# Kernel optimization log

Measured on AMD Instinct MI355X. Metric: run time of the kernel, lower is better.

## Reference

```python
import jax, jax.numpy as jnp
import numpy as np

B, K, C, D, L, H, FF = 64, 1024, 512, 256, 2, 4, 1024
DH = D // H
EPS = 1e-5
NEG = -jnp.inf
SCALE = 1.0 / float(np.sqrt(DH))


def _ln(x, w, b):
    m = x.mean(-1, keepdims=True)
    v = ((x - m) ** 2).mean(-1, keepdims=True)
    return (x - m) * jax.lax.rsqrt(v + EPS) * w + b


def _star_attn(x, key_pad, pad_c, Wq, bq, Wk, bk, Wv, bv, Wo, bo):
    # Star topology: rows 0,1 (query,dustbin) attend to all non-padded keys;
    # each candidate row attends only to {query, dustbin, itself}.
    Bb, S, _ = x.shape
    q = (x @ Wq.T + bq).reshape(Bb, S, H, DH)
    k = (x @ Wk.T + bk).reshape(Bb, S, H, DH)
    v = (x @ Wv.T + bv).reshape(Bb, S, H, DH)
    # global rows
    qg = q[:, :2]
    sg = jnp.einsum('bthd,bshd->bhts', qg, k) * SCALE            # [B,H,2,S]
    sg = jnp.where(key_pad[:, None, None, :], NEG, sg)
    out_g = jnp.einsum('bhts,bshd->bthd', jax.nn.softmax(sg, -1), v)  # [B,2,H,DH]
    # candidate rows: scores against the 2 global keys + self key
    qc, kc, vc = q[:, 2:], k[:, 2:], v[:, 2:]
    kg, vg = k[:, :2], v[:, :2]
    s2 = jnp.einsum('bkhd,bthd->bkht', qc, kg) * SCALE           # [B,K,H,2]
    ss = jnp.einsum('bkhd,bkhd->bkh', qc, kc) * SCALE            # [B,K,H]
    ss = jnp.where(pad_c[:, :, None], NEG, ss)                   # padded self-key disallowed
    w = jax.nn.softmax(jnp.concatenate([s2, ss[..., None]], -1), -1)  # [B,K,H,3]
    out_c = jnp.einsum('bkht,bthd->bkhd', w[..., :2], vg) + w[..., 2:] * vc
    out = jnp.concatenate([out_g, out_c], 1).reshape(Bb, S, D)
    return out @ Wo.T + bo


def _forward(query, candidates, candidate_mask, qp_w, qp_b, cp_w, cp_b,
             dustbin, type_emb, ln1_w, ln1_b, ln2_w, ln2_b,
             Wq, bq, Wk, bk, Wv, bv, Wo, bo,
             ff1_w, ff1_b, ff2_w, ff2_b, head_ln_w, head_ln_b, head_w, head_b):
    Bb = query.shape[0]
    qt = (query @ qp_w.T + qp_b + type_emb[0])[:, None]          # [B,1,D]
    dt = jnp.broadcast_to(dustbin + type_emb[1], (Bb, 1, D))
    ct = candidates @ cp_w.T + cp_b + type_emb[2]                # [B,K,D]
    x = jnp.concatenate([qt, dt, ct], 1)                         # [B,K+2,D]
    pad_c = jnp.logical_not(candidate_mask)
    key_pad = jnp.concatenate([jnp.zeros((Bb, 2), bool), pad_c], 1)
    for l in range(L):  # pre-LN encoder layers (norm_first, eval so dropout=0)
        x = x + _star_attn(_ln(x, ln1_w[l], ln1_b[l]), key_pad, pad_c,
                           Wq[l], bq[l], Wk[l], bk[l], Wv[l], bv[l], Wo[l], bo[l])
        h = _ln(x, ln2_w[l], ln2_b[l])
        x = x + (jax.nn.gelu(h @ ff1_w[l].T + ff1_b[l], approximate=False) @ ff2_w[l].T + ff2_b[l])
    logits = (_ln(x, head_ln_w, head_ln_b) @ head_w.T + head_b)[..., 0]  # [B,K+2]
    cand = jnp.where(candidate_mask, logits[:, 2:], NEG)
    return jnp.concatenate([logits[:, 1:2], cand], 1)            # [B,K+1]


def setup_inputs() -> dict:
    key = jax.random.key(0)
    ks = iter(jax.random.split(key, 40))
    n = lambda shape, s=0.02: jax.random.normal(next(ks), shape, jnp.float32) * s
    return dict(
        query=jax.random.normal(next(ks), (B, C), jnp.float32),
        candidates=jax.random.normal(next(ks), (B, K, C), jnp.float32),
        candidate_mask=jax.random.bernoulli(next(ks), 0.9, (B, K)),
        qp_w=n((D, C)), qp_b=jnp.zeros(D),
        cp_w=n((D, C)), cp_b=jnp.zeros(D),
        dustbin=n((D,)), type_emb=n((3, D)),
        ln1_w=jnp.ones((L, D)), ln1_b=jnp.zeros((L, D)),
        ln2_w=jnp.ones((L, D)), ln2_b=jnp.zeros((L, D)),
        Wq=n((L, D, D)), bq=jnp.zeros((L, D)),
        Wk=n((L, D, D)), bk=jnp.zeros((L, D)),
        Wv=n((L, D, D)), bv=jnp.zeros((L, D)),
        Wo=n((L, D, D)), bo=jnp.zeros((L, D)),
        ff1_w=n((L, FF, D)), ff1_b=jnp.zeros((L, FF)),
        ff2_w=n((L, D, FF)), ff2_b=jnp.zeros((L, D)),
        head_ln_w=jnp.ones(D), head_ln_b=jnp.zeros(D),
        head_w=n((1, D)), head_b=jnp.zeros(1),
    )


def reference(query, candidates, candidate_mask, qp_w, qp_b, cp_w, cp_b,
              dustbin, type_emb, ln1_w, ln1_b, ln2_w, ln2_b,
              Wq, bq, Wk, bk, Wv, bv, Wo, bo,
              ff1_w, ff1_b, ff2_w, ff2_b, head_ln_w, head_ln_b, head_w, head_b):
    return _forward(query, candidates, candidate_mask, qp_w, qp_b, cp_w, cp_b,
                    dustbin, type_emb, ln1_w, ln1_b, ln2_w, ln2_b,
                    Wq, bq, Wk, bk, Wv, bv, Wo, bo,
                    ff1_w, ff1_b, ff2_w, ff2_b, head_ln_w, head_ln_b, head_w, head_b)
```

## Files before the change

kernel.cpp:

```cpp
#include <hip/hip_runtime.h>
#include <math.h>

static constexpr int Bc = 64;
static constexpr int Kc = 1024;
static constexpr int Cc = 512;
static constexpr int Dc = 256;
static constexpr int Hc = 4;
static constexpr int Sc = 1026;
static constexpr int FFc = 1024;
static constexpr float EPSc = 1e-5f;
static constexpr float SCALEc = 0.125f;
static constexpr float NEG_OUT = -1.0e30f;

typedef __attribute__((ext_vector_type(8))) short short8;
typedef __attribute__((ext_vector_type(8))) unsigned short u16x8;
typedef __attribute__((ext_vector_type(4))) float f32x4;

__device__ __forceinline__ float bf2f(unsigned short u) {
  union { float f; unsigned int i; } c; c.i = ((unsigned int)u) << 16; return c.f;
}
__device__ __forceinline__ unsigned short f2bf(float f) {
  union { float f; unsigned int i; } c; c.f = f;
  unsigned int i = c.i;
  unsigned int r = (i + 0x7fffu + ((i >> 16) & 1u)) >> 16;
  return (unsigned short)r;
}
__device__ __forceinline__ unsigned int cvt_pk_bf16(float a, float b) {
  unsigned int d;
  asm("v_cvt_pk_bf16_f32 %0, %1, %2" : "=v"(d) : "v"(a), "v"(b));
  return d;
}

__device__ __forceinline__ float wave_sum(float v) {
#pragma unroll
  for (int off = 32; off > 0; off >>= 1) v += __shfl_xor(v, off, 64);
  return v;
}
__device__ __forceinline__ float wave_max(float v) {
#pragma unroll
  for (int off = 32; off > 0; off >>= 1) v = fmaxf(v, __shfl_xor(v, off, 64));
  return v;
}

__device__ __forceinline__ void async_ld16(const unsigned short* g, unsigned short* l) {
  __builtin_amdgcn_global_load_lds(
      (const __attribute__((address_space(1))) void*)g,
      (__attribute__((address_space(3))) void*)l, 16, 0, 0);
}

__device__ __forceinline__ float gelu_fast(float u) {
  const float z = 1.5957691216057308f * u * (1.0f + 0.044715f * u * u);
  return u / (1.0f + __expf(-z));
}

template <int EPI, int MAP, int CASTA>
__global__ __launch_bounds__(256) void gemm_mfma(
    const void* __restrict__ Av, const unsigned short* __restrict__ W,
    const float* __restrict__ bias, const void* extra,
    void* Cout, int N, int Kd, int ldc, int MB, int NB) {
  __shared__ unsigned short lds[16384];
  const int xcd = blockIdx.x & 7;
  const int slot = blockIdx.x >> 3;
  const int nb = slot % NB;
  const int mb = (slot / NB) * 8 + xcd;
  if (mb >= MB) return;
  const int m0 = mb * 128;
  const int n0 = nb * 128;
  const int tid = threadIdx.x;
  const int w = tid >> 6;
  const int lane = tid & 63;

  const unsigned short* A = (const unsigned short*)Av;
  const float* Af = (const float*)Av;

  const int srA[2] = {(w * 2 + 0) * 16 + (lane >> 2), (w * 2 + 1) * 16 + (lane >> 2)};
  const unsigned short* pA[2];
  const unsigned short* pB[2];
#pragma unroll
  for (int c = 0; c < 2; ++c) {
    const int kc = ((lane & 3) ^ ((srA[c] >> 1) & 3)) * 8;
    if (!CASTA) pA[c] = A + (size_t)(m0 + srA[c]) * Kd + kc;
    pB[c] = W + (size_t)(n0 + srA[c]) * Kd + kc;
  }
  const int lreg0 = (w * 2 + 0) * 512;
  const int lreg1 = (w * 2 + 1) * 512;

  f32x4 zero = {0.f, 0.f, 0.f, 0.f};
  f32x4 acc[4][4];
#pragma unroll
  for (int i = 0; i < 4; ++i)
#pragma unroll
    for (int j = 0; j < 4; ++j) acc[i][j] = zero;

  const int mrow = (w & 1) * 64;
  const int nrow = (w >> 1) * 64;
  const int l15 = lane & 15;
  const int quad = lane >> 4;
  const int koff = (quad ^ ((l15 >> 1) & 3)) * 16;

  auto stage = [&](int kk, int b) {
    if (CASTA) {
#pragma unroll
      for (int wi = 0; wi < 4; ++wi) {
        const int g = wi * 256 + tid;
        const int row = g >> 3;
        const int k4 = g & 7;
        const int phys =
            row * 32 + ((((k4 >> 1) ^ ((row >> 1) & 3))) << 3) + ((k4 & 1) << 2);
        const float4 a4 =
            *(const float4*)(Af + (size_t)(m0 + row) * Kd + kk + k4 * 4);
        uint2 o;
        o.x = cvt_pk_bf16(a4.x, a4.y);
        o.y = cvt_pk_bf16(a4.z, a4.w);
        *(uint2*)(&lds[b * 4096 + phys]) = o;
      }
    } else {
      async_ld16(pA[0] + kk, &lds[b * 4096 + lreg0]);
      async_ld16(pA[1] + kk, &lds[b * 4096 + lreg1]);
    }
    async_ld16(pB[0] + kk, &lds[8192 + b * 4096 + lreg0]);
    async_ld16(pB[1] + kk, &lds[8192 + b * 4096 + lreg1]);
  };

  const int niter = Kd >> 5;
  stage(0, 0);
  for (int it = 0; it < niter; ++it) {
    const int cur = it & 1;
    __syncthreads();
    if (it + 1 < niter) stage((it + 1) << 5, cur ^ 1);
    const char* AsB = (const char*)&lds[cur * 4096];
    const char* WsB = (const char*)&lds[8192 + cur * 4096];
    short8 af[4], bfr[4];
#pragma unroll
    for (int i = 0; i < 4; ++i)
      af[i] = *(const short8*)(AsB + (size_t)(mrow + i * 16 + l15) * 64 + koff);
#pragma unroll
    for (int j = 0; j < 4; ++j)
      bfr[j] = *(const short8*)(WsB + (size_t)(nrow + j * 16 + l15) * 64 + koff);
#pragma unroll
    for (int i = 0; i < 4; ++i)
#pragma unroll
      for (int j = 0; j < 4; ++j)
        acc[i][j] = __builtin_amdgcn_mfma_f32_16x16x32_bf16(bfr[j], af[i],
                                                            acc[i][j], 0, 0, 0);
  }

  const float* extraF = (const float*)extra;
  const unsigned short* extraB = (const unsigned short*)extra;
  float4 bj[4];
#pragma unroll
  for (int j = 0; j < 4; ++j) {
    const int n = n0 + nrow + j * 16 + quad * 4;
    float4 t4 = *(const float4*)(bias + n);
    if (EPI == 1) {
      const float4 e4 = *(const float4*)(extraF + n);
      t4.x += e4.x; t4.y += e4.y; t4.z += e4.z; t4.w += e4.w;
    }
    bj[j] = t4;
  }
  __syncthreads();
#pragma unroll
  for (int i = 0; i < 4; ++i) {
    const int m = mrow + i * 16 + l15;
    const int swz = (m & 7) << 1;
#pragma unroll
    for (int j = 0; j < 4; ++j) {
      float v0 = acc[i][j][0] + bj[j].x;
      float v1 = acc[i][j][1] + bj[j].y;
      float v2 = acc[i][j][2] + bj[j].z;
      float v3 = acc[i][j][3] + bj[j].w;
      if (EPI == 3) {
        v0 = gelu_fast(v0); v1 = gelu_fast(v1);
        v2 = gelu_fast(v2); v3 = gelu_fast(v3);
      }
      uint2 pk;
      pk.x = cvt_pk_bf16(v0, v1);
      pk.y = cvt_pk_bf16(v2, v3);
      const int g = ((nrow + j * 16 + quad * 4) >> 2) ^ swz;
      *(uint2*)(&lds[m * 128 + g * 4]) = pk;
    }
  }
  __syncthreads();
  unsigned short* outb = (unsigned short*)Cout;
#pragma unroll
  for (int c8 = 0; c8 < 8; ++c8) {
    const int idx = c8 * 256 + tid;
    const int row = idx >> 4;
    const int cc = idx & 15;
    const int gsr = (2 * cc) ^ ((row & 7) << 1);
    u16x8 val = *(const u16x8*)(&lds[row * 128 + gsr * 4]);
    const int col = cc * 8;
    const int m = m0 + row;
    const size_t orow =
        (MAP == 1) ? ((size_t)(m >> 10) * Sc + 2 + (m & 1023)) : (size_t)m;
    const size_t go = orow * (size_t)ldc + n0 + col;
    if (EPI == 2) {
      u16x8 rv = *(const u16x8*)(extraB + go);
      unsigned int* vp = (unsigned int*)&val;
#pragma unroll
      for (int e = 0; e < 4; ++e) {
        const float a0 = bf2f(val[2 * e]) + bf2f(rv[2 * e]);
        const float a1 = bf2f(val[2 * e + 1]) + bf2f(rv[2 * e + 1]);
        vp[e] = cvt_pk_bf16(a0, a1);
      }
    }
    *(u16x8*)(outb + go) = val;
  }
}

struct CastTab {
  const float* src[10];
  unsigned short* dst[10];
  int n4[10];
};
__global__ __launch_bounds__(256) void cast_multi(CastTab t) {
  const int e = blockIdx.y;
  const int n4 = t.n4[e];
  const float4* s = (const float4*)t.src[e];
  uint2* d = (uint2*)t.dst[e];
  for (int i = blockIdx.x * 256 + threadIdx.x; i < n4; i += gridDim.x * 256) {
    float4 f = s[i];
    uint2 o;
    o.x = cvt_pk_bf16(f.x, f.y);
    o.y = cvt_pk_bf16(f.z, f.w);
    d[i] = o;
  }
}

__global__ __launch_bounds__(256) void bias_concat(const float* bq, const float* bk,
                                                   const float* bv, float* qkvb) {
  const int i = blockIdx.x * 256 + threadIdx.x;
  if (i >= 2 * 768) return;
  const int l = i / 768;
  const int j = i - l * 768;
  float v;
  if (j < 256) v = bq[l * 256 + j];
  else if (j < 512) v = bk[l * 256 + j - 256];
  else v = bv[l * 256 + j - 512];
  qkvb[i] = v;
}

__global__ __launch_bounds__(256) void embed_qd(
    const float* __restrict__ qin, const float* __restrict__ qp_w,
    const float* __restrict__ qp_b, const float* __restrict__ dustbin,
    const float* __restrict__ type_emb, unsigned short* __restrict__ x) {
  const int b = blockIdx.x;
  const int d = threadIdx.x;
  __shared__ __align__(16) float qs[512];
  qs[d] = qin[b * 512 + d];
  qs[d + 256] = qin[b * 512 + 256 + d];
  __syncthreads();
  float acc = 0.0f;
  const float* wr = qp_w + (size_t)d * 512;
#pragma unroll 4
  for (int c = 0; c < 512; c += 4) {
    float4 w4 = *(const float4*)(wr + c);
    acc = fmaf(qs[c], w4.x, acc);
    acc = fmaf(qs[c + 1], w4.y, acc);
    acc = fmaf(qs[c + 2], w4.z, acc);
    acc = fmaf(qs[c + 3], w4.w, acc);
  }
  const size_t base = (size_t)b * Sc * Dc;
  x[base + d] = f2bf(acc + qp_b[d] + type_emb[d]);
  x[base + Dc + d] = f2bf(dustbin[d] + type_emb[Dc + d]);
}

__global__ __launch_bounds__(256) void ln_kernel(
    const unsigned short* __restrict__ x, const float* __restrict__ w,
    const float* __restrict__ b, unsigned short* __restrict__ y, int nrows) {
  const int wave = threadIdx.x >> 6;
  const int lane = threadIdx.x & 63;
  const int row = blockIdx.x * 4 + wave;
  if (row >= nrows) return;
  const unsigned short* xr = x + (size_t)row * Dc;
  ushort4 xv = *(const ushort4*)(xr + lane * 4);
  const float v0 = bf2f(xv.x), v1 = bf2f(xv.y), v2 = bf2f(xv.z), v3 = bf2f(xv.w);
  float s = v0 + v1 + v2 + v3;
  float sq = v0 * v0 + v1 * v1 + v2 * v2 + v3 * v3;
  s = wave_sum(s);
  sq = wave_sum(sq);
  const float mean = s * (1.0f / Dc);
  const float var = sq * (1.0f / Dc) - mean * mean;
  const float rs = rsqrtf(var + EPSc);
  float4 wv = *(const float4*)(w + lane * 4);
  float4 bv = *(const float4*)(b + lane * 4);
  uint2 o;
  o.x = cvt_pk_bf16((v0 - mean) * rs * wv.x + bv.x,
                    (v1 - mean) * rs * wv.y + bv.y);
  o.y = cvt_pk_bf16((v2 - mean) * rs * wv.z + bv.z,
                    (v3 - mean) * rs * wv.w + bv.w);
  *(uint2*)(y + (size_t)row * Dc + lane * 4) = o;
}

__global__ __launch_bounds__(256) void attn_global(
    const unsigned short* __restrict__ qkv, const unsigned char* __restrict__ mask,
    unsigned short* __restrict__ ao) {
  const int b = blockIdx.x;
  const int h = blockIdx.y;
  const int tid = threadIdx.x;
  const int wv = tid >> 6;
  const int lane = tid & 63;
  __shared__ float q0s[64], q1s[64];
  __shared__ float sc0[Sc], sc1[Sc];
  __shared__ float rbuf[4][2];
  __shared__ float obuf[2][4][64];
  const size_t base = (size_t)b * Sc * 768 + h * 64;
  if (tid < 64) {
    q0s[tid] = bf2f(qkv[base + tid]);
    q1s[tid] = bf2f(qkv[base + 768 + tid]);
  }
  __syncthreads();

  float lm0 = -INFINITY, lm1 = -INFINITY;
  for (int s = tid; s < Sc; s += 256) {
    const unsigned short* kr = qkv + base + 256 + (size_t)s * 768;
    float d0 = 0.0f, d1 = 0.0f;
#pragma unroll
    for (int c = 0; c < 64; c += 8) {
      u16x8 kv = *(const u16x8*)(kr + c);
#pragma unroll
      for (int e = 0; e < 8; ++e) {
        const float kf = bf2f(kv[e]);
        d0 = fmaf(q0s[c + e], kf, d0);
        d1 = fmaf(q1s[c + e], kf, d1);
      }
    }
    const bool pad = (s >= 2) && (mask[b * Kc + (s - 2)] == 0);
    const float s0 = pad ? -INFINITY : d0 * SCALEc;
    const float s1 = pad ? -INFINITY : d1 * SCALEc;
    sc0[s] = s0; sc1[s] = s1;
    lm0 = fmaxf(lm0, s0); lm1 = fmaxf(lm1, s1);
  }
  lm0 = wave_max(lm0);
  lm1 = wave_max(lm1);
  if (lane == 0) { rbuf[wv][0] = lm0; rbuf[wv][1] = lm1; }
  __syncthreads();
  const float m0 = fmaxf(fmaxf(rbuf[0][0], rbuf[1][0]), fmaxf(rbuf[2][0], rbuf[3][0]));
  const float m1 = fmaxf(fmaxf(rbuf[0][1], rbuf[1][1]), fmaxf(rbuf[2][1], rbuf[3][1]));
  float ls0 = 0.0f, ls1 = 0.0f;
  for (int s = tid; s < Sc; s += 256) {
    const float e0 = expf(sc0[s] - m0);
    const float e1 = expf(sc1[s] - m1);
    sc0[s] = e0; sc1[s] = e1;
    ls0 += e0; ls1 += e1;
  }
  ls0 = wave_sum(ls0);
  ls1 = wave_sum(ls1);
  __syncthreads();
  if (lane == 0) { rbuf[wv][0] = ls0; rbuf[wv][1] = ls1; }
  __syncthreads();
  const float t0 = rbuf[0][0] + rbuf[1][0] + rbuf[2][0] + rbuf[3][0];
  const float t1 = rbuf[0][1] + rbuf[1][1] + rbuf[2][1] + rbuf[3][1];
  float o0 = 0.0f, o1 = 0.0f;
  for (int s = wv; s < Sc; s += 4) {
    const float vvv = bf2f(qkv[base + 512 + (size_t)s * 768 + lane]);
    o0 = fmaf(sc0[s], vvv, o0);
    o1 = fmaf(sc1[s], vvv, o1);
  }
  obuf[0][wv][lane] = o0;
  obuf[1][wv][lane] = o1;
  __syncthreads();
  if (wv == 0) {
    const float a0 = obuf[0][0][lane] + obuf[0][1][lane] + obuf[0][2][lane] + obuf[0][3][lane];
    const float a1 = obuf[1][0][lane] + obuf[1][1][lane] + obuf[1][2][lane] + obuf[1][3][lane];
    const size_t ob = ((size_t)b * Sc) * Dc + h * 64;
    ao[ob + lane] = f2bf(a0 / t0);
    ao[ob + Dc + lane] = f2bf(a1 / t1);
  }
}

__global__ __launch_bounds__(256) void attn_cand(
    const unsigned short* __restrict__ qkv, const unsigned char* __restrict__ mask,
    unsigned short* __restrict__ ao) {
  const int bk = blockIdx.x;
  const int b = bk >> 10;
  const int kk = bk & 1023;
  const int h = threadIdx.x >> 6;
  const int lane = threadIdx.x & 63;
  const size_t rowg = (size_t)b * Sc * 768 + h * 64;
  const size_t rowc = rowg + (size_t)(2 + kk) * 768;
  const float qc = bf2f(qkv[rowc + lane]);
  float p0 = qc * bf2f(qkv[rowg + 256 + lane]);
  float p1 = qc * bf2f(qkv[rowg + 256 + 768 + lane]);
  float p2 = qc * bf2f(qkv[rowc + 256 + lane]);
#pragma unroll
  for (int off = 32; off > 0; off >>= 1) {
    p0 += __shfl_xor(p0, off, 64);
    p1 += __shfl_xor(p1, off, 64);
    p2 += __shfl_xor(p2, off, 64);
  }
  const bool pad = (mask[b * Kc + kk] == 0);
  const float s0 = p0 * SCALEc;
  const float s1 = p1 * SCALEc;
  const float s2 = pad ? -INFINITY : p2 * SCALEc;
  const float m = fmaxf(fmaxf(s0, s1), s2);
  const float e0 = expf(s0 - m);
  const float e1 = expf(s1 - m);
  const float e2 = pad ? 0.0f : expf(s2 - m);
  const float inv = 1.0f / (e0 + e1 + e2);
  const float o = (e0 * bf2f(qkv[rowg + 512 + lane]) +
                   e1 * bf2f(qkv[rowg + 512 + 768 + lane]) +
                   e2 * bf2f(qkv[rowc + 512 + lane])) * inv;
  ao[((size_t)b * Sc + 2 + kk) * Dc + h * 64 + lane] = f2bf(o);
}

__global__ __launch_bounds__(256) void head_kernel(
    const unsigned short* __restrict__ x, const float* __restrict__ lnw,
    const float* __restrict__ lnb, const float* __restrict__ hw,
    const float* __restrict__ hb, const unsigned char* __restrict__ mask,
    float* __restrict__ out) {
  const int gw = blockIdx.x * 4 + (threadIdx.x >> 6);
  const int lane = threadIdx.x & 63;
  if (gw >= Bc * 1025) return;
  const int b = gw / 1025;
  const int j = gw - b * 1025;
  const int s = 1 + j;
  const unsigned short* xr = x + ((size_t)b * Sc + s) * Dc;
  ushort4 xv = *(const ushort4*)(xr + lane * 4);
  const float v0 = bf2f(xv.x), v1 = bf2f(xv.y), v2 = bf2f(xv.z), v3 = bf2f(xv.w);
  float su = v0 + v1 + v2 + v3;
  float sq = v0 * v0 + v1 * v1 + v2 * v2 + v3 * v3;
  su = wave_sum(su);
  sq = wave_sum(sq);
  const float mean = su * (1.0f / Dc);
  const float var = sq * (1.0f / Dc) - mean * mean;
  const float rs = rsqrtf(var + EPSc);
  float4 wv = *(const float4*)(lnw + lane * 4);
  float4 bv = *(const float4*)(lnb + lane * 4);
  float4 hv = *(const float4*)(hw + lane * 4);
  float d = ((v0 - mean) * rs * wv.x + bv.x) * hv.x +
            ((v1 - mean) * rs * wv.y + bv.y) * hv.y +
            ((v2 - mean) * rs * wv.z + bv.z) * hv.z +
            ((v3 - mean) * rs * wv.w + bv.w) * hv.w;
  d = wave_sum(d);
  if (lane == 0) {
    const float logit = d + hb[0];
    float res;
    if (j == 0) res = logit;
    else res = (mask[b * Kc + (j - 1)] != 0) ? logit : NEG_OUT;
    out[(size_t)b * 1025 + j] = res;
  }
}

extern "C" void kernel_launch(void* const* d_in, const int* in_sizes, int n_in,
                              void* d_out, int out_size, void* d_ws,
                              size_t ws_size, hipStream_t stream) {
  const float* query = (const float*)d_in[0];
  const float* cands = (const float*)d_in[1];
  const unsigned char* mask = (const unsigned char*)d_in[2];
  const float* qp_w = (const float*)d_in[3];
  const float* qp_b = (const float*)d_in[4];
  const float* cp_w = (const float*)d_in[5];
  const float* cp_b = (const float*)d_in[6];
  const float* dustbin = (const float*)d_in[7];
  const float* type_emb = (const float*)d_in[8];
  const float* ln1_w = (const float*)d_in[9];
  const float* ln1_b = (const float*)d_in[10];
  const float* ln2_w = (const float*)d_in[11];
  const float* ln2_b = (const float*)d_in[12];
  const float* Wq = (const float*)d_in[13];
  const float* bq = (const float*)d_in[14];
  const float* Wk = (const float*)d_in[15];
  const float* bk = (const float*)d_in[16];
  const float* Wv = (const float*)d_in[17];
  const float* bv = (const float*)d_in[18];
  const float* Wo = (const float*)d_in[19];
  const float* bo = (const float*)d_in[20];
  const float* f1w = (const float*)d_in[21];
  const float* f1b = (const float*)d_in[22];
  const float* f2w = (const float*)d_in[23];
  const float* f2b = (const float*)d_in[24];
  const float* hlw = (const float*)d_in[25];
  const float* hlb = (const float*)d_in[26];
  const float* hw = (const float*)d_in[27];
  const float* hb = (const float*)d_in[28];
  float* out = (float*)d_out;

  const size_t XSZ = (size_t)Bc * Sc * Dc;
  const size_t FFSZ = (size_t)Bc * Sc * FFc;

  char* p = (char*)d_ws;
  unsigned short* x = (unsigned short*)p;   p += XSZ * 2;
  unsigned short* y = (unsigned short*)p;   p += XSZ * 2;
  unsigned short* ao = (unsigned short*)p;  p += XSZ * 2;
  unsigned short* big = (unsigned short*)p; p += FFSZ * 2;
  unsigned short* qkv = big;
  unsigned short* ff = big;
  unsigned short* cpw_b = (unsigned short*)p;
  unsigned short* qkvw_b = cpw_b + 131072;
  unsigned short* Wo_b = qkvw_b + 2 * 768 * 256;
  unsigned short* f1_b = Wo_b + 131072;
  unsigned short* f2_b = f1_b + 524288;
  float* qkvb = (float*)(f2_b + 524288);

  const int BS = Bc * Sc;
  auto sgrid = [](int MB, int NB) { return (unsigned)(NB * (((MB + 7) >> 3) << 3)); };

  CastTab t;
  t.src[0] = cp_w;  t.dst[0] = cpw_b; t.n4[0] = 131072 / 4;
  t.src[1] = Wo;    t.dst[1] = Wo_b;  t.n4[1] = 131072 / 4;
  t.src[2] = f1w;   t.dst[2] = f1_b;  t.n4[2] = 524288 / 4;
  t.src[3] = f2w;   t.dst[3] = f2_b;  t.n4[3] = 524288 / 4;
  for (int l = 0; l < 2; ++l) {
    t.src[4 + l * 3 + 0] = Wq + l * 65536;
    t.src[4 + l * 3 + 1] = Wk + l * 65536;
    t.src[4 + l * 3 + 2] = Wv + l * 65536;
    t.dst[4 + l * 3 + 0] = qkvw_b + l * 196608 + 0 * 65536;
    t.dst[4 + l * 3 + 1] = qkvw_b + l * 196608 + 1 * 65536;
    t.dst[4 + l * 3 + 2] = qkvw_b + l * 196608 + 2 * 65536;
    t.n4[4 + l * 3 + 0] = 65536 / 4;
    t.n4[4 + l * 3 + 1] = 65536 / 4;
    t.n4[4 + l * 3 + 2] = 65536 / 4;
  }
  cast_multi<<<dim3(128, 10), 256, 0, stream>>>(t);
  bias_concat<<<6, 256, 0, stream>>>(bq, bk, bv, qkvb);

  gemm_mfma<1, 1, 1><<<sgrid(512, 2), 256, 0, stream>>>(
      cands, cpw_b, cp_b, type_emb + 2 * Dc, x, Dc, Cc, Dc, 512, 2);
  embed_qd<<<Bc, 256, 0, stream>>>(query, qp_w, qp_b, dustbin, type_emb, x);

  for (int l = 0; l < 2; ++l) {
    ln_kernel<<<BS / 4, 256, 0, stream>>>(x, ln1_w + l * Dc, ln1_b + l * Dc, y, BS);
    gemm_mfma<4, 0, 0><<<sgrid(513, 6), 256, 0, stream>>>(
        y, qkvw_b + l * 196608, qkvb + l * 768, nullptr, qkv, 768, Dc, 768, 513, 6);
    attn_global<<<dim3(Bc, Hc), 256, 0, stream>>>(qkv, mask, ao);
    attn_cand<<<Bc * Kc, 256, 0, stream>>>(qkv, mask, ao);
    gemm_mfma<2, 0, 0><<<sgrid(513, 2), 256, 0, stream>>>(
        ao, Wo_b + l * 65536, bo + l * Dc, x, x, Dc, Dc, Dc, 513, 2);
    ln_kernel<<<BS / 4, 256, 0, stream>>>(x, ln2_w + l * Dc, ln2_b + l * Dc, y, BS);
    gemm_mfma<3, 0, 0><<<sgrid(513, 8), 256, 0, stream>>>(
        y, f1_b + l * 524288 / 2, f1b + l * FFc, nullptr, ff, FFc, Dc, FFc, 513, 8);
    gemm_mfma<2, 0, 0><<<sgrid(513, 2), 256, 0, stream>>>(
        ff, f2_b + l * 524288 / 2, f2b + l * Dc, x, x, Dc, FFc, Dc, 513, 2);
  }

  head_kernel<<<(Bc * 1025 + 3) / 4, 256, 0, stream>>>(x, hlw, hlb, hw, hb, mask, out);
}
```

Before: 1.037 ms.

## Fuse FF1+GELU+FF2 into one kernel keeping hidden activations in LDS

Result: slower. 1.773 ms (+71.0%).

```diff
diff --git a/kernel.cpp b/kernel.cpp
--- a/kernel.cpp
+++ b/kernel.cpp
@@ -49,8 +49,8 @@
 }
 
 __device__ __forceinline__ float gelu_fast(float u) {
-  const float z = 1.5957691216057308f * u * (1.0f + 0.044715f * u * u);
-  return u / (1.0f + __expf(-z));
+  const float z = u * fmaf(u * u, 0.07135481627f, 1.5957691216f);
+  return __fdividef(u, 1.0f + __expf(-z));
 }
 
 template <int EPI, int MAP, int CASTA>
@@ -205,6 +205,125 @@
       }
     }
     *(u16x8*)(outb + go) = val;
+  }
+}
+
+__global__ __launch_bounds__(512, 2) void ff_fused(
+    const unsigned short* __restrict__ A,
+    const unsigned short* __restrict__ W1,
+    const float* __restrict__ b1,
+    const unsigned short* __restrict__ W2,
+    const float* __restrict__ b2,
+    unsigned short* __restrict__ X) {
+  __shared__ __align__(16) unsigned short hbuf[2][128 * 64];
+  const int m0 = blockIdx.x * 128;
+  const int tid = threadIdx.x;
+  const int w = tid >> 6;
+  const int lane = tid & 63;
+  const int l15 = lane & 15;
+  const int quad = lane >> 4;
+  const int wm = w >> 1;
+  const int wn = w & 1;
+
+  short8 areg[2][8];
+  {
+    const unsigned short* ap0 =
+        A + (size_t)(m0 + wm * 32 + l15) * 256 + quad * 8;
+#pragma unroll
+    for (int i = 0; i < 2; ++i)
+#pragma unroll
+      for (int ks = 0; ks < 8; ++ks)
+        areg[i][ks] = *(const short8*)(ap0 + i * 16 * 256 + ks * 32);
+  }
+
+  const f32x4 zero = {0.f, 0.f, 0.f, 0.f};
+  f32x4 acc2[2][8];
+#pragma unroll
+  for (int i = 0; i < 2; ++i)
+#pragma unroll
+    for (int j = 0; j < 8; ++j) acc2[i][j] = zero;
+
+  const int swz0 = ((wm * 32 + l15) & 7) << 1;
+  const int swz1 = ((wm * 32 + 16 + l15) & 7) << 1;
+
+  for (int c = 0; c < 16; ++c) {
+    f32x4 acc1[2][2];
+#pragma unroll
+    for (int i = 0; i < 2; ++i)
+#pragma unroll
+      for (int j = 0; j < 2; ++j) acc1[i][j] = zero;
+    const unsigned short* w1p =
+        W1 + (size_t)(c * 64 + wn * 32 + l15) * 256 + quad * 8;
+#pragma unroll
+    for (int ks = 0; ks < 8; ++ks) {
+      const short8 wf0 = *(const short8*)(w1p + ks * 32);
+      const short8 wf1 = *(const short8*)(w1p + 16 * 256 + ks * 32);
+      acc1[0][0] = __builtin_amdgcn_mfma_f32_16x16x32_bf16(wf0, areg[0][ks], acc1[0][0], 0, 0, 0);
+      acc1[0][1] = __builtin_amdgcn_mfma_f32_16x16x32_bf16(wf1, areg[0][ks], acc1[0][1], 0, 0, 0);
+      acc1[1][0] = __builtin_amdgcn_mfma_f32_16x16x32_bf16(wf0, areg[1][ks], acc1[1][0], 0, 0, 0);
+      acc1[1][1] = __builtin_amdgcn_mfma_f32_16x16x32_bf16(wf1, areg[1][ks], acc1[1][1], 0, 0, 0);
+    }
+    unsigned short* hb = hbuf[c & 1];
+#pragma unroll
+    for (int i = 0; i < 2; ++i) {
+      const int m = wm * 32 + i * 16 + l15;
+      const int swz = (i == 0) ? swz0 : swz1;
+#pragma unroll
+      for (int j = 0; j < 2; ++j) {
+        const float4 bb =
+            *(const float4*)(b1 + c * 64 + wn * 32 + j * 16 + quad * 4);
+        const float v0 = gelu_fast(acc1[i][j][0] + bb.x);
+        const float v1 = gelu_fast(acc1[i][j][1] + bb.y);
+        const float v2 = gelu_fast(acc1[i][j][2] + bb.z);
+        const float v3 = gelu_fast(acc1[i][j][3] + bb.w);
+        uint2 pk;
+        pk.x = cvt_pk_bf16(v0, v1);
+        pk.y = cvt_pk_bf16(v2, v3);
+        const int g = ((wn * 32 + j * 16 + quad * 4) >> 2) ^ swz;
+        *(uint2*)(&hb[m * 64 + g * 4]) = pk;
+      }
+    }
+    __syncthreads();
+    const unsigned short* w2p =
+        W2 + (size_t)(wn * 128 + l15) * 1024 + c * 64 + quad * 8;
+#pragma unroll
+    for (int ks2 = 0; ks2 < 2; ++ks2) {
+      short8 hf[2];
+#pragma unroll
+      for (int i = 0; i < 2; ++i) {
+        const int m = wm * 32 + i * 16 + l15;
+        const int swz = (i == 0) ? swz0 : swz1;
+        const int g = ((ks2 * 32 + quad * 8) >> 2) ^ swz;
+        hf[i] = *(const short8*)(&hb[m * 64 + g * 4]);
+      }
+#pragma unroll
+      for (int j = 0; j < 8; ++j) {
+        const short8 wf2 = *(const short8*)(w2p + (size_t)(j * 16) * 1024 + ks2 * 32);
+#pragma unroll
+        for (int i = 0; i < 2; ++i)
+          acc2[i][j] = __builtin_amdgcn_mfma_f32_16x16x32_bf16(wf2, hf[i], acc2[i][j], 0, 0, 0);
+      }
+    }
+  }
+
+#pragma unroll
+  for (int i = 0; i < 2; ++i) {
+    const int m = m0 + wm * 32 + i * 16 + l15;
+    unsigned short* xr = X + (size_t)m * 256 + wn * 128;
+#pragma unroll
+    for (int j = 0; j < 8; ++j) {
+      const int n = j * 16 + quad * 4;
+      const float4 bb = *(const float4*)(b2 + wn * 128 + n);
+      const uint2 rv = *(const uint2*)(xr + n);
+      const float v0 = acc2[i][j][0] + bb.x + bf2f((unsigned short)(rv.x & 0xffff));
+      const float v1 = acc2[i][j][1] + bb.y + bf2f((unsigned short)(rv.x >> 16));
+      const float v2 = acc2[i][j][2] + bb.z + bf2f((unsigned short)(rv.y & 0xffff));
+      const float v3 = acc2[i][j][3] + bb.w + bf2f((unsigned short)(rv.y >> 16));
+      uint2 pk;
+      pk.x = cvt_pk_bf16(v0, v1);
+      pk.y = cvt_pk_bf16(v2, v3);
+      *(uint2*)(xr + n) = pk;
+    }
   }
 }
 
@@ -485,7 +604,6 @@
   unsigned short* ao = (unsigned short*)p;  p += XSZ * 2;
   unsigned short* big = (unsigned short*)p; p += FFSZ * 2;
   unsigned short* qkv = big;
-  unsigned short* ff = big;
   unsigned short* cpw_b = (unsigned short*)p;
   unsigned short* qkvw_b = cpw_b + 131072;
   unsigned short* Wo_b = qkvw_b + 2 * 768 * 256;
@@ -528,10 +646,8 @@
     gemm_mfma<2, 0, 0><<<sgrid(513, 2), 256, 0, stream>>>(
         ao, Wo_b + l * 65536, bo + l * Dc, x, x, Dc, Dc, Dc, 513, 2);
     ln_kernel<<<BS / 4, 256, 0, stream>>>(x, ln2_w + l * Dc, ln2_b + l * Dc, y, BS);
-    gemm_mfma<3, 0, 0><<<sgrid(513, 8), 256, 0, stream>>>(
-        y, f1_b + l * 524288 / 2, f1b + l * FFc, nullptr, ff, FFc, Dc, FFc, 513, 8);
-    gemm_mfma<2, 0, 0><<<sgrid(513, 2), 256, 0, stream>>>(
-        ff, f2_b + l * 524288 / 2, f2b + l * Dc, x, x, Dc, FFc, Dc, 513, 2);
+    ff_fused<<<513, 512, 0, stream>>>(
+        y, f1_b + l * 262144, f1b + l * FFc, f2_b + l * 262144, f2b + l * Dc, x);
   }
 
   head_kernel<<<(Bc * 1025 + 3) / 4, 256, 0, stream>>>(x, hlw, hlb, hw, hb, mask, out);
```
